# Performance work log

Measured on AMD Instinct MI355X. Metric: run time of the kernel, lower is better.

Reference implementation:

```python
import jax, jax.numpy as jnp
import numpy as np

B, T = 32, 4096
ATTN_DIM, ENC_DIM, DEC_DIM = 128, 512, 1024


def setup_inputs() -> dict:
    key = jax.random.key(0)
    k1, k2, k3, k4, k5, k6 = jax.random.split(key, 6)
    return {
        "query": jax.random.normal(k1, (B, DEC_DIM), dtype=jnp.float32),
        "memory": jax.random.normal(k2, (B, T, ENC_DIM), dtype=jnp.float32),
        "attention_weights_cum": jax.random.uniform(k3, (B, T), dtype=jnp.float32),
        "Wq": jax.random.normal(k4, (DEC_DIM, ATTN_DIM), dtype=jnp.float32) * (1.0 / np.sqrt(DEC_DIM)),
        "Wm": jax.random.normal(k5, (ENC_DIM, ATTN_DIM), dtype=jnp.float32) * (1.0 / np.sqrt(ENC_DIM)),
        "v": jax.random.normal(k6, (ATTN_DIM,), dtype=jnp.float32),
    }


def reference(query, memory, attention_weights_cum, Wq, Wm, v):
    # processed_query: [B, 1, A]; processed_memory: [B, T, A]
    pq = jnp.einsum('bd,da->ba', query, Wq)[:, None, :]
    pm = jnp.einsum('bte,ea->bta', memory, Wm)
    # scores: [B, T] = sum_a tanh(pq + pm) * v
    scores = jnp.einsum('bta,a->bt', jnp.tanh(pq + pm), v)
    alignments = jax.nn.softmax(scores, axis=-1)  # [B, T]
    context = jnp.einsum('bt,bte->be', alignments, memory)  # [B, E]
    return context, alignments
```

## Files before the change

### kernel.cpp

```cpp
#include <hip/hip_runtime.h>
#include <hip/hip_bf16.h>
#include <math.h>

#define B_SZ 32
#define T_SZ 4096
#define A_SZ 128
#define E_SZ 512
#define D_SZ 1024
#define NCH  32

typedef __attribute__((ext_vector_type(8))) short short8;
typedef __attribute__((ext_vector_type(4))) float f32x4;

static __device__ __forceinline__ unsigned short f32_to_bf16_rne(float x) {
    unsigned int u = __float_as_uint(x);
    unsigned int r = (u + 0x7fffu + ((u >> 16) & 1u)) >> 16;
    return (unsigned short)r;
}
static __device__ __forceinline__ float bf16_to_f32(unsigned short h) {
    return __uint_as_float(((unsigned int)h) << 16);
}
static __device__ __forceinline__ float tanh_fast(float x) {
    float ax = fabsf(x);
    float e  = __expf(2.f * ax);
    float r  = 1.f - 2.f / (e + 1.f);
    return __builtin_copysignf(r, x);
}

__global__ __launch_bounds__(256) void k_prep(const float* __restrict__ q,
                                              const float* __restrict__ Wq,
                                              const float* __restrict__ Wm,
                                              float* __restrict__ pq,
                                              unsigned short* __restrict__ WmTh,
                                              unsigned short* __restrict__ WmTl) {
    const int tid = threadIdx.x;
    if (blockIdx.x < 32) {
        const int b = blockIdx.x;
        __shared__ float ql[D_SZ];
        #pragma unroll
        for (int s = 0; s < D_SZ / 256; ++s)
            ql[s * 256 + tid] = q[b * D_SZ + s * 256 + tid];
        __syncthreads();
        if (tid < A_SZ) {
            const int a = tid;
            float acc = 0.f;
            #pragma unroll 8
            for (int d = 0; d < D_SZ; ++d)
                acc = fmaf(ql[d], Wq[d * A_SZ + a], acc);
            pq[b * A_SZ + a] = acc;
        }
    } else {
        const int a = blockIdx.x - 32;
        for (int e = tid; e < E_SZ; e += 256) {
            float x = Wm[(size_t)e * A_SZ + a];
            unsigned short h = f32_to_bf16_rne(x);
            float r = x - bf16_to_f32(h);
            unsigned short l = f32_to_bf16_rne(r);
            WmTh[(size_t)a * E_SZ + e] = h;
            WmTl[(size_t)a * E_SZ + e] = l;
        }
    }
}

#define AST 36
#define BST 40

__global__ __launch_bounds__(256, 4) void k_fused(
    const float* __restrict__ mem,
    const unsigned short* __restrict__ WmTh,
    const unsigned short* __restrict__ WmTl,
    const float* __restrict__ pq,
    const float* __restrict__ v,
    float* __restrict__ scores_raw,
    float* __restrict__ ctx_part,
    float* __restrict__ mZ)
{
    __shared__ unsigned short Ah[128 * AST];
    __shared__ unsigned short Al[128 * AST];
    __shared__ unsigned short Bh[128 * BST];
    __shared__ unsigned short Bl[128 * BST];
    __shared__ float sc[128];
    __shared__ float wbuf[128];
    __shared__ float red[8];

    const int cb = blockIdx.x;
    const int b  = blockIdx.y;
    const int t0 = cb * 128;
    const int tid = threadIdx.x;
    const int w = tid >> 6;
    const int lane = tid & 63;
    const int l16 = lane & 15;
    const int lk = lane >> 4;

    const float* memB = mem + ((size_t)b * T_SZ + t0) * E_SZ;

    float pqr[8], vr[8];
    #pragma unroll
    for (int n = 0; n < 8; ++n) {
        pqr[n] = pq[b * A_SZ + n * 16 + l16];
        vr[n]  = v[n * 16 + l16];
    }

    f32x4 acc[2][8];
    #pragma unroll
    for (int m = 0; m < 2; ++m)
        #pragma unroll
        for (int n = 0; n < 8; ++n)
            acc[m][n] = (f32x4){0.f, 0.f, 0.f, 0.f};

    for (int c = 0; c < 16; ++c) {
        const int e0 = c * 32;
        __syncthreads();
        #pragma unroll
        for (int s = 0; s < 4; ++s) {
            int idx = s * 256 + tid;
            int row = idx >> 3;
            int e4  = (idx & 7) << 2;
            float4 val = *(const float4*)(memB + (size_t)row * E_SZ + e0 + e4);
            float xs[4] = {val.x, val.y, val.z, val.w};
            unsigned short h[4], l[4];
            #pragma unroll
            for (int k = 0; k < 4; ++k) {
                h[k] = f32_to_bf16_rne(xs[k]);
                l[k] = f32_to_bf16_rne(xs[k] - bf16_to_f32(h[k]));
            }
            unsigned int hp0 = (unsigned int)h[0] | ((unsigned int)h[1] << 16);
            unsigned int hp1 = (unsigned int)h[2] | ((unsigned int)h[3] << 16);
            unsigned int lp0 = (unsigned int)l[0] | ((unsigned int)l[1] << 16);
            unsigned int lp1 = (unsigned int)l[2] | ((unsigned int)l[3] << 16);
            *(uint2*)&Ah[row * AST + e4] = make_uint2(hp0, hp1);
            *(uint2*)&Al[row * AST + e4] = make_uint2(lp0, lp1);
        }
        #pragma unroll
        for (int s = 0; s < 2; ++s) {
            int idx = s * 256 + tid;
            int a   = idx >> 2;
            int es  = (idx & 3) << 3;
            *(short8*)&Bh[a * BST + es] =
                *(const short8*)&WmTh[(size_t)a * E_SZ + e0 + es];
            *(short8*)&Bl[a * BST + es] =
                *(const short8*)&WmTl[(size_t)a * E_SZ + e0 + es];
        }
        __syncthreads();

        short8 ah[2], al[2];
        #pragma unroll
        for (int m = 0; m < 2; ++m) {
            int off = (w * 32 + m * 16 + l16) * AST + lk * 8;
            ah[m] = *(const short8*)&Ah[off];
            al[m] = *(const short8*)&Al[off];
        }
        #pragma unroll
        for (int n = 0; n < 8; ++n) {
            int boff = (n * 16 + l16) * BST + lk * 8;
            short8 bh = *(const short8*)&Bh[boff];
            short8 bl = *(const short8*)&Bl[boff];
            acc[0][n] = __builtin_amdgcn_mfma_f32_16x16x32_bf16(ah[0], bh, acc[0][n], 0, 0, 0);
            acc[1][n] = __builtin_amdgcn_mfma_f32_16x16x32_bf16(ah[1], bh, acc[1][n], 0, 0, 0);
            acc[0][n] = __builtin_amdgcn_mfma_f32_16x16x32_bf16(al[0], bh, acc[0][n], 0, 0, 0);
            acc[1][n] = __builtin_amdgcn_mfma_f32_16x16x32_bf16(al[1], bh, acc[1][n], 0, 0, 0);
            acc[0][n] = __builtin_amdgcn_mfma_f32_16x16x32_bf16(ah[0], bl, acc[0][n], 0, 0, 0);
            acc[1][n] = __builtin_amdgcn_mfma_f32_16x16x32_bf16(ah[1], bl, acc[1][n], 0, 0, 0);
        }
    }

    #pragma unroll
    for (int m = 0; m < 2; ++m) {
        float part[4] = {0.f, 0.f, 0.f, 0.f};
        #pragma unroll
        for (int n = 0; n < 8; ++n)
            #pragma unroll
            for (int r = 0; r < 4; ++r)
                part[r] += tanh_fast(pqr[n] + acc[m][n][r]) * vr[n];
        #pragma unroll
        for (int r = 0; r < 4; ++r) {
            #pragma unroll
            for (int off = 1; off < 16; off <<= 1)
                part[r] += __shfl_xor(part[r], off);
        }
        if (l16 == 0) {
            const int tl = w * 32 + m * 16 + lk * 4;
            #pragma unroll
            for (int r = 0; r < 4; ++r)
                sc[tl + r] = part[r];
        }
    }
    __syncthreads();

    float mv = sc[tid & 127];
    #pragma unroll
    for (int off = 1; off < 64; off <<= 1)
        mv = fmaxf(mv, __shfl_xor(mv, off));
    if (lane == 0) red[w] = mv;
    __syncthreads();
    const float Mc = fmaxf(fmaxf(red[0], red[1]), fmaxf(red[2], red[3]));

    float wv = 0.f;
    if (tid < 128) {
        wv = __expf(sc[tid] - Mc);
        wbuf[tid] = wv;
        scores_raw[(size_t)b * T_SZ + t0 + tid] = sc[tid];
    }
    float sv = wv;
    #pragma unroll
    for (int off = 1; off < 64; off <<= 1)
        sv += __shfl_xor(sv, off);
    if (lane == 0) red[4 + w] = sv;
    __syncthreads();
    if (tid == 0) {
        const float Zc = red[4] + red[5];
        mZ[(b * NCH + cb) * 2 + 0] = Mc;
        mZ[(b * NCH + cb) * 2 + 1] = Zc;
    }

    const int e2 = tid * 2;
    float2 a2 = make_float2(0.f, 0.f);
    #pragma unroll 8
    for (int t = 0; t < 128; ++t) {
        float2 mm = *(const float2*)(memB + (size_t)t * E_SZ + e2);
        const float wt = wbuf[t];
        a2.x = fmaf(wt, mm.x, a2.x);
        a2.y = fmaf(wt, mm.y, a2.y);
    }
    *(float2*)(ctx_part + ((size_t)cb * B_SZ + b) * E_SZ + e2) = a2;
}

__global__ __launch_bounds__(256) void k_combine(
    const float* __restrict__ ctx_part,
    const float* __restrict__ mZ,
    float* __restrict__ ctx,
    float* __restrict__ align)
{
    const int b = blockIdx.x;
    const int tid = threadIdx.x;
    float mc[NCH], zc[NCH], ec[NCH];
    float M = -1e30f;
    #pragma unroll
    for (int c = 0; c < NCH; ++c) {
        float2 p = *(const float2*)(mZ + (b * NCH + c) * 2);
        mc[c] = p.x; zc[c] = p.y;
        M = fmaxf(M, p.x);
    }
    float Z = 0.f;
    #pragma unroll
    for (int c = 0; c < NCH; ++c) {
        ec[c] = __expf(mc[c] - M);
        Z = fmaf(zc[c], ec[c], Z);
    }
    const float invZ = 1.f / Z;

    const int e2 = tid * 2;
    float2 a2 = make_float2(0.f, 0.f);
    #pragma unroll
    for (int c = 0; c < NCH; ++c) {
        float2 p = *(const float2*)(ctx_part + ((size_t)c * B_SZ + b) * E_SZ + e2);
        a2.x = fmaf(p.x, ec[c], a2.x);
        a2.y = fmaf(p.y, ec[c], a2.y);
    }
    float2 outv = make_float2(a2.x * invZ, a2.y * invZ);
    *(float2*)(ctx + (size_t)b * E_SZ + e2) = outv;

    float* row = align + (size_t)b * T_SZ;
    #pragma unroll
    for (int s = 0; s < 4; ++s) {
        float4 vv = *(float4*)&row[(s * 256 + tid) * 4];
        vv.x = __expf(vv.x - M) * invZ;
        vv.y = __expf(vv.y - M) * invZ;
        vv.z = __expf(vv.z - M) * invZ;
        vv.w = __expf(vv.w - M) * invZ;
        *(float4*)&row[(s * 256 + tid) * 4] = vv;
    }
}

extern "C" void kernel_launch(void* const* d_in, const int* in_sizes, int n_in,
                              void* d_out, int out_size, void* d_ws, size_t ws_size,
                              hipStream_t stream) {
    const float* query  = (const float*)d_in[0];
    const float* memory = (const float*)d_in[1];
    const float* Wq     = (const float*)d_in[3];
    const float* Wm     = (const float*)d_in[4];
    const float* v      = (const float*)d_in[5];

    float* ctx_out   = (float*)d_out;
    float* align_out = (float*)d_out + B_SZ * E_SZ;

    char* ws = (char*)d_ws;
    float*          pq       = (float*)(ws + 0);
    unsigned short* WmTh     = (unsigned short*)(ws + 16384);
    unsigned short* WmTl     = (unsigned short*)(ws + 147456);
    float*          mZ       = (float*)(ws + 278528);
    float*          ctx_part = (float*)(ws + 286720);

    k_prep<<<160, 256, 0, stream>>>(query, Wq, Wm, pq, WmTh, WmTl);
    k_fused<<<dim3(NCH, B_SZ), 256, 0, stream>>>(memory, WmTh, WmTl, pq, v,
                                                 align_out, ctx_part, mZ);
    k_combine<<<B_SZ, 256, 0, stream>>>(ctx_part, mZ, ctx_out, align_out);
}
```

Measured before the change: 501.8 us.

## Prefetch next memory chunk into registers and rotate chunk order per block

The main GEMM loop now loads the next 32-column chunk of memory into registers while the current chunk is converted and multiplied, software-pipelining global loads against MFMA work. The chunk order is rotated per block by (cb+b)&15 so that concurrent blocks read different Wm slices and memory columns. The pq/v register loads move after the loop to free registers during the main loop. The prefetch raises register pressure, which may reduce occupancy.

```diff
diff --git a/kernel.cpp b/kernel.cpp
--- a/kernel.cpp
+++ b/kernel.cpp
@@ -91,15 +91,12 @@
     const int lane = tid & 63;
     const int l16 = lane & 15;
     const int lk = lane >> 4;
+    const int rot = (cb + b) & 15;
 
     const float* memB = mem + ((size_t)b * T_SZ + t0) * E_SZ;
 
-    float pqr[8], vr[8];
-    #pragma unroll
-    for (int n = 0; n < 8; ++n) {
-        pqr[n] = pq[b * A_SZ + n * 16 + l16];
-        vr[n]  = v[n * 16 + l16];
-    }
+    const int ar0 = tid >> 3;
+    const int ae4 = (tid & 7) << 2;
 
     f32x4 acc[2][8];
     #pragma unroll
@@ -108,16 +105,49 @@
         for (int n = 0; n < 8; ++n)
             acc[m][n] = (f32x4){0.f, 0.f, 0.f, 0.f};
 
+    float4 ra[4];
+    {
+        const int e0 = rot * 32;
+        #pragma unroll
+        for (int s = 0; s < 4; ++s)
+            ra[s] = *(const float4*)(memB + (size_t)(ar0 + s * 32) * E_SZ + e0 + ae4);
+    }
+
     for (int c = 0; c < 16; ++c) {
-        const int e0 = c * 32;
-        __syncthreads();
+        const int cc = (c + rot) & 15;
+        const int e0 = cc * 32;
+
+        short8 rbh[2], rbl[2];
+        #pragma unroll
+        for (int s = 0; s < 2; ++s) {
+            int idx = s * 256 + tid;
+            int a   = idx >> 2;
+            int es  = (idx & 3) << 3;
+            rbh[s] = *(const short8*)&WmTh[(size_t)a * E_SZ + e0 + es];
+            rbl[s] = *(const short8*)&WmTl[(size_t)a * E_SZ + e0 + es];
+        }
+
+        float4 rn[4];
+        if (c < 15) {
+            const int en = ((c + 1 + rot) & 15) * 32;
+            #pragma unroll
+            for (int s = 0; s < 4; ++s)
+                rn[s] = *(const float4*)(memB + (size_t)(ar0 + s * 32) * E_SZ + en + ae4);
+        }
+
+        #pragma unroll
+        for (int s = 0; s < 2; ++s) {
+            int idx = s * 256 + tid;
+            int a   = idx >> 2;
+            int es  = (idx & 3) << 3;
+            *(short8*)&Bh[a * BST + es] = rbh[s];
+            *(short8*)&Bl[a * BST + es] = rbl[s];
+        }
+
         #pragma unroll
         for (int s = 0; s < 4; ++s) {
-            int idx = s * 256 + tid;
-            int row = idx >> 3;
-            int e4  = (idx & 7) << 2;
-            float4 val = *(const float4*)(memB + (size_t)row * E_SZ + e0 + e4);
-            float xs[4] = {val.x, val.y, val.z, val.w};
+            const int row = ar0 + s * 32;
+            float xs[4] = {ra[s].x, ra[s].y, ra[s].z, ra[s].w};
             unsigned short h[4], l[4];
             #pragma unroll
             for (int k = 0; k < 4; ++k) {
@@ -128,18 +158,8 @@
             unsigned int hp1 = (unsigned int)h[2] | ((unsigned int)h[3] << 16);
             unsigned int lp0 = (unsigned int)l[0] | ((unsigned int)l[1] << 16);
             unsigned int lp1 = (unsigned int)l[2] | ((unsigned int)l[3] << 16);
-            *(uint2*)&Ah[row * AST + e4] = make_uint2(hp0, hp1);
-            *(uint2*)&Al[row * AST + e4] = make_uint2(lp0, lp1);
-        }
-        #pragma unroll
-        for (int s = 0; s < 2; ++s) {
-            int idx = s * 256 + tid;
-            int a   = idx >> 2;
-            int es  = (idx & 3) << 3;
-            *(short8*)&Bh[a * BST + es] =
-                *(const short8*)&WmTh[(size_t)a * E_SZ + e0 + es];
-            *(short8*)&Bl[a * BST + es] =
-                *(const short8*)&WmTl[(size_t)a * E_SZ + e0 + es];
+            *(uint2*)&Ah[row * AST + ae4] = make_uint2(hp0, hp1);
+            *(uint2*)&Al[row * AST + ae4] = make_uint2(lp0, lp1);
         }
         __syncthreads();
 
@@ -162,8 +182,20 @@
             acc[0][n] = __builtin_amdgcn_mfma_f32_16x16x32_bf16(ah[0], bl, acc[0][n], 0, 0, 0);
             acc[1][n] = __builtin_amdgcn_mfma_f32_16x16x32_bf16(ah[1], bl, acc[1][n], 0, 0, 0);
         }
-    }
-
+        __syncthreads();
+
+        if (c < 15) {
+            #pragma unroll
+            for (int s = 0; s < 4; ++s) ra[s] = rn[s];
+        }
+    }
+
+    float pqr[8], vr[8];
+    #pragma unroll
+    for (int n = 0; n < 8; ++n) {
+        pqr[n] = pq[b * A_SZ + n * 16 + l16];
+        vr[n]  = v[n * 16 + l16];
+    }
     #pragma unroll
     for (int m = 0; m < 2; ++m) {
         float part[4] = {0.f, 0.f, 0.f, 0.f};
```

Result: faster. 468.3 us (-6.7%).

## Load MFMA operands directly from global memory with register double-buffering, drop LDS staging

Applied to the files above, without the earlier changes.

The score GEMM no longer stages memory and Wm tiles through shared memory behind barriers. Each lane now loads its own A fragments (fp32, split into bf16 hi/lo in registers) and the B fragments straight from global memory, double-buffering the next E chunk in registers. It also rotates the starting E chunk per block to spread cache/channel traffic, and switches the hi/lo split from round-to-nearest to truncation. The cost is more register pressure (occupancy hint lowered from 4 to 3), uncoalesced per-lane global loads of Wm that rely on cache, and slightly different rounding of the split.

```diff
diff --git a/kernel.cpp b/kernel.cpp
--- a/kernel.cpp
+++ b/kernel.cpp
@@ -11,6 +11,9 @@
 
 typedef __attribute__((ext_vector_type(8))) short short8;
 typedef __attribute__((ext_vector_type(4))) float f32x4;
+typedef __attribute__((ext_vector_type(4))) unsigned int u32x4;
+
+union cvt8 { u32x4 u; short8 s; };
 
 static __device__ __forceinline__ unsigned short f32_to_bf16_rne(float x) {
     unsigned int u = __float_as_uint(x);
@@ -25,6 +28,22 @@
     float e  = __expf(2.f * ax);
     float r  = 1.f - 2.f / (e + 1.f);
     return __builtin_copysignf(r, x);
+}
+
+static __device__ __forceinline__ void split8(const float4 x0, const float4 x1,
+                                              short8& hi, short8& lo) {
+    float xs[8] = {x0.x, x0.y, x0.z, x0.w, x1.x, x1.y, x1.z, x1.w};
+    cvt8 h, l;
+    #pragma unroll
+    for (int j = 0; j < 4; ++j) {
+        unsigned int u0 = __float_as_uint(xs[2 * j]);
+        unsigned int u1 = __float_as_uint(xs[2 * j + 1]);
+        h.u[j] = (u0 >> 16) | (u1 & 0xffff0000u);
+        float lo0 = xs[2 * j]     - __uint_as_float(u0 & 0xffff0000u);
+        float lo1 = xs[2 * j + 1] - __uint_as_float(u1 & 0xffff0000u);
+        l.u[j] = (__float_as_uint(lo0) >> 16) | (__float_as_uint(lo1) & 0xffff0000u);
+    }
+    hi = h.s; lo = l.s;
 }
 
 __global__ __launch_bounds__(256) void k_prep(const float* __restrict__ q,
@@ -62,10 +81,7 @@
     }
 }
 
-#define AST 36
-#define BST 40
-
-__global__ __launch_bounds__(256, 4) void k_fused(
+__global__ __launch_bounds__(256, 3) void k_fused(
     const float* __restrict__ mem,
     const unsigned short* __restrict__ WmTh,
     const unsigned short* __restrict__ WmTl,
@@ -75,10 +91,6 @@
     float* __restrict__ ctx_part,
     float* __restrict__ mZ)
 {
-    __shared__ unsigned short Ah[128 * AST];
-    __shared__ unsigned short Al[128 * AST];
-    __shared__ unsigned short Bh[128 * BST];
-    __shared__ unsigned short Bl[128 * BST];
     __shared__ float sc[128];
     __shared__ float wbuf[128];
     __shared__ float red[8];
@@ -91,15 +103,13 @@
     const int lane = tid & 63;
     const int l16 = lane & 15;
     const int lk = lane >> 4;
+    const int rot = (cb + b) & 15;
 
     const float* memB = mem + ((size_t)b * T_SZ + t0) * E_SZ;
 
-    float pqr[8], vr[8];
-    #pragma unroll
-    for (int n = 0; n < 8; ++n) {
-        pqr[n] = pq[b * A_SZ + n * 16 + l16];
-        vr[n]  = v[n * 16 + l16];
-    }
+    const float* aBase = memB + (size_t)(w * 32 + l16) * E_SZ + lk * 8;
+    const unsigned short* bhBase = WmTh + (size_t)l16 * E_SZ + lk * 8;
+    const unsigned short* blBase = WmTl + (size_t)l16 * E_SZ + lk * 8;
 
     f32x4 acc[2][8];
     #pragma unroll
@@ -108,62 +118,67 @@
         for (int n = 0; n < 8; ++n)
             acc[m][n] = (f32x4){0.f, 0.f, 0.f, 0.f};
 
-    for (int c = 0; c < 16; ++c) {
-        const int e0 = c * 32;
-        __syncthreads();
-        #pragma unroll
-        for (int s = 0; s < 4; ++s) {
-            int idx = s * 256 + tid;
-            int row = idx >> 3;
-            int e4  = (idx & 7) << 2;
-            float4 val = *(const float4*)(memB + (size_t)row * E_SZ + e0 + e4);
-            float xs[4] = {val.x, val.y, val.z, val.w};
-            unsigned short h[4], l[4];
-            #pragma unroll
-            for (int k = 0; k < 4; ++k) {
-                h[k] = f32_to_bf16_rne(xs[k]);
-                l[k] = f32_to_bf16_rne(xs[k] - bf16_to_f32(h[k]));
-            }
-            unsigned int hp0 = (unsigned int)h[0] | ((unsigned int)h[1] << 16);
-            unsigned int hp1 = (unsigned int)h[2] | ((unsigned int)h[3] << 16);
-            unsigned int lp0 = (unsigned int)l[0] | ((unsigned int)l[1] << 16);
-            unsigned int lp1 = (unsigned int)l[2] | ((unsigned int)l[3] << 16);
-            *(uint2*)&Ah[row * AST + e4] = make_uint2(hp0, hp1);
-            *(uint2*)&Al[row * AST + e4] = make_uint2(lp0, lp1);
-        }
-        #pragma unroll
-        for (int s = 0; s < 2; ++s) {
-            int idx = s * 256 + tid;
-            int a   = idx >> 2;
-            int es  = (idx & 3) << 3;
-            *(short8*)&Bh[a * BST + es] =
-                *(const short8*)&WmTh[(size_t)a * E_SZ + e0 + es];
-            *(short8*)&Bl[a * BST + es] =
-                *(const short8*)&WmTl[(size_t)a * E_SZ + e0 + es];
-        }
-        __syncthreads();
-
-        short8 ah[2], al[2];
-        #pragma unroll
-        for (int m = 0; m < 2; ++m) {
-            int off = (w * 32 + m * 16 + l16) * AST + lk * 8;
-            ah[m] = *(const short8*)&Ah[off];
-            al[m] = *(const short8*)&Al[off];
-        }
-        #pragma unroll
-        for (int n = 0; n < 8; ++n) {
-            int boff = (n * 16 + l16) * BST + lk * 8;
-            short8 bh = *(const short8*)&Bh[boff];
-            short8 bl = *(const short8*)&Bl[boff];
-            acc[0][n] = __builtin_amdgcn_mfma_f32_16x16x32_bf16(ah[0], bh, acc[0][n], 0, 0, 0);
-            acc[1][n] = __builtin_amdgcn_mfma_f32_16x16x32_bf16(ah[1], bh, acc[1][n], 0, 0, 0);
-            acc[0][n] = __builtin_amdgcn_mfma_f32_16x16x32_bf16(al[0], bh, acc[0][n], 0, 0, 0);
-            acc[1][n] = __builtin_amdgcn_mfma_f32_16x16x32_bf16(al[1], bh, acc[1][n], 0, 0, 0);
-            acc[0][n] = __builtin_amdgcn_mfma_f32_16x16x32_bf16(ah[0], bl, acc[0][n], 0, 0, 0);
-            acc[1][n] = __builtin_amdgcn_mfma_f32_16x16x32_bf16(ah[1], bl, acc[1][n], 0, 0, 0);
-        }
-    }
-
+    #define E0(cc) ((((cc) + rot) & 15) * 32)
+
+    #define LOADA(P, e0_) {                                                   \
+        _Pragma("unroll")                                                     \
+        for (int m = 0; m < 2; ++m) {                                         \
+            const float* p_ = aBase + (size_t)m * 16 * E_SZ + (e0_);          \
+            P[m][0] = *(const float4*)p_;                                     \
+            P[m][1] = *(const float4*)(p_ + 4);                               \
+        }                                                                     \
+    }
+
+    #define COMPUTE(P, e0_) {                                                 \
+        short8 ah0, al0, ah1, al1;                                            \
+        split8(P[0][0], P[0][1], ah0, al0);                                   \
+        split8(P[1][0], P[1][1], ah1, al1);                                   \
+        short8 cbh[2][2], cbl[2][2];                                          \
+        const size_t nstep = (size_t)16 * E_SZ;                               \
+        cbh[0][0] = *(const short8*)(bhBase + (e0_));                         \
+        cbh[0][1] = *(const short8*)(bhBase + nstep + (e0_));                 \
+        cbl[0][0] = *(const short8*)(blBase + (e0_));                         \
+        cbl[0][1] = *(const short8*)(blBase + nstep + (e0_));                 \
+        _Pragma("unroll")                                                     \
+        for (int j = 0; j < 4; ++j) {                                         \
+            const int cur = j & 1;                                            \
+            if (j < 3) {                                                      \
+                const size_t off = (size_t)(2 * (j + 1)) * 16 * E_SZ + (e0_); \
+                cbh[cur ^ 1][0] = *(const short8*)(bhBase + off);             \
+                cbh[cur ^ 1][1] = *(const short8*)(bhBase + off + nstep);     \
+                cbl[cur ^ 1][0] = *(const short8*)(blBase + off);             \
+                cbl[cur ^ 1][1] = *(const short8*)(blBase + off + nstep);     \
+            }                                                                 \
+            _Pragma("unroll")                                                 \
+            for (int q = 0; q < 2; ++q) {                                     \
+                const int n = 2 * j + q;                                      \
+                short8 bh = cbh[cur][q], bl = cbl[cur][q];                    \
+                acc[0][n] = __builtin_amdgcn_mfma_f32_16x16x32_bf16(ah0, bh, acc[0][n], 0, 0, 0); \
+                acc[1][n] = __builtin_amdgcn_mfma_f32_16x16x32_bf16(ah1, bh, acc[1][n], 0, 0, 0); \
+                acc[0][n] = __builtin_amdgcn_mfma_f32_16x16x32_bf16(al0, bh, acc[0][n], 0, 0, 0); \
+                acc[1][n] = __builtin_amdgcn_mfma_f32_16x16x32_bf16(al1, bh, acc[1][n], 0, 0, 0); \
+                acc[0][n] = __builtin_amdgcn_mfma_f32_16x16x32_bf16(ah0, bl, acc[0][n], 0, 0, 0); \
+                acc[1][n] = __builtin_amdgcn_mfma_f32_16x16x32_bf16(ah1, bl, acc[1][n], 0, 0, 0); \
+            }                                                                 \
+        }                                                                     \
+    }
+
+    float4 pA[2][2], pB[2][2];
+    LOADA(pA, E0(0));
+
+    for (int c = 0; c < 16; c += 2) {
+        LOADA(pB, E0(c + 1));
+        COMPUTE(pA, E0(c));
+        if (c + 2 < 16) LOADA(pA, E0(c + 2));
+        COMPUTE(pB, E0(c + 1));
+    }
+
+    float pqr[8], vr[8];
+    #pragma unroll
+    for (int n = 0; n < 8; ++n) {
+        pqr[n] = pq[b * A_SZ + n * 16 + l16];
+        vr[n]  = v[n * 16 + l16];
+    }
     #pragma unroll
     for (int m = 0; m < 2; ++m) {
         float part[4] = {0.f, 0.f, 0.f, 0.f};
@@ -223,6 +238,10 @@
         a2.y = fmaf(wt, mm.y, a2.y);
     }
     *(float2*)(ctx_part + ((size_t)cb * B_SZ + b) * E_SZ + e2) = a2;
+
+    #undef E0
+    #undef LOADA
+    #undef COMPUTE
 }
 
 __global__ __launch_bounds__(256) void k_combine(
```

Measured after the change: 603.6 us. 1.2x slower.
